# Optimization experiments

Hardware: AMD Instinct MI355X
Metric: run time of the kernel (lower is better)

## Reference

```python
import jax, jax.numpy as jnp
import numpy as np

H, DK = 16, 64
F = H * DK  # n_feat = 1024
B, T = 2, 2048


def setup_inputs() -> dict:
    key = jax.random.key(0)
    ks = jax.random.split(key, 11)
    mk = lambda k, sh: jax.random.normal(k, sh, dtype=jnp.float32)
    inp = {
        "query": mk(ks[0], (B, T, F)),
        "key": mk(ks[1], (B, T, F)),
        "value": mk(ks[2], (B, T, F)),
    }
    # Standard RoPE frequency table, shaped [T,1,1,DK] to broadcast over [t,b,h,d].
    pos = jnp.arange(T, dtype=jnp.float32)[:, None]
    inv_freq = 1.0 / (10000.0 ** (jnp.arange(0, DK, 2, dtype=jnp.float32) / DK))
    ang = pos * inv_freq                       # [T, DK/2]
    emb = jnp.concatenate([ang, ang], axis=-1)  # [T, DK]
    inp["cos"] = jnp.cos(emb)[:, None, None, :]
    inp["sin"] = jnp.sin(emb)[:, None, None, :]
    scale = 1.0 / np.sqrt(F).astype(np.float32)
    for i, n in enumerate(["wq", "wk", "wv", "wo"]):
        inp[n] = mk(ks[3 + i], (F, F)) * scale  # torch Linear weight layout [out,in]
    for i, n in enumerate(["bq", "bk", "bv", "bo"]):
        inp[n] = mk(ks[7 + i], (F,)) * 0.01
    return inp


def _rtt_half(x):
    d = x.shape[-1]
    return jnp.concatenate([-x[..., d // 2:], x[..., :d // 2]], axis=-1)


def reference(query, key, value, cos, sin, wq, bq, wk, bk, wv, bv, wo, bo):
    b, t, f = query.shape
    h, d = H, DK
    # [b,t,f] -> [t,b,h,d] as in the torch code (RoPE applied pre-projection)
    to_tbhd = lambda x: jnp.swapaxes(x, 0, 1).reshape(t, b, h, d)
    q = to_tbhd(query)
    k = to_tbhd(key)
    c, s = cos[:t], sin[:t]
    q = q * c + _rtt_half(q) * s
    k = k * c + _rtt_half(k) * s
    back = lambda x: jnp.swapaxes(x.reshape(t, b, f), 0, 1)  # -> [b,t,f]
    q, k = back(q), back(k)
    lin = lambda x, w, bias: x @ w.T + bias
    Q = lin(q, wq, bq).reshape(b, t, h, d)
    K = lin(k, wk, bk).reshape(b, t, h, d)
    V = lin(value, wv, bv).reshape(b, t, h, d)
    scores = jnp.einsum('bqhd,bkhd->bhqk', Q, K) / jnp.sqrt(jnp.float32(d))
    attn = jax.nn.softmax(scores, axis=-1)
    o = jnp.einsum('bhqk,bkhd->bqhd', attn, V).reshape(b, t, f)
    return o @ wo.T + bo
```

## Files before the change

### kernel.cpp

```cpp
#include <hip/hip_runtime.h>
#include <hip/hip_bf16.h>

#define DEVI __device__ __forceinline__

typedef unsigned short u16;
typedef unsigned int u32;
typedef __attribute__((ext_vector_type(8))) short bf16x8;
typedef __attribute__((ext_vector_type(4))) short bf16x4;
typedef __attribute__((ext_vector_type(4))) float f32x4;

#define Bn 2
#define Tn 2048
#define Hn 16
#define Dn 64
#define Fn 1024

DEVI u16 tobf(float f) {
    __hip_bfloat16 h = __float2bfloat16(f);
    return __builtin_bit_cast(u16, h);
}
DEVI float frombf(u16 u) {
    return __builtin_bit_cast(float, ((u32)u) << 16);
}

DEVI f32x4 mfma16(bf16x8 a, bf16x8 b, f32x4 c) {
    return __builtin_amdgcn_mfma_f32_16x16x32_bf16(a, b, c, 0, 0, 0);
}

DEVI void gload_lds16(const u16* g, u16* l) {
    __builtin_amdgcn_global_load_lds(
        (const __attribute__((address_space(1))) void*)g,
        (__attribute__((address_space(3))) void*)l, 16, 0, 0);
}

__global__ __launch_bounds__(256) void k_prep(const float* __restrict__ q,
                                              const float* __restrict__ k,
                                              const float* __restrict__ v,
                                              const float* __restrict__ cosb,
                                              const float* __restrict__ sinb,
                                              const float* __restrict__ wq,
                                              const float* __restrict__ wk,
                                              const float* __restrict__ wv,
                                              const float* __restrict__ wo,
                                              u16* __restrict__ Aq,
                                              u16* __restrict__ Ak,
                                              u16* __restrict__ Av) {
    if (blockIdx.x < 4096) {
        unsigned idx = blockIdx.x * 256 + threadIdx.x;
        unsigned which = idx >> 19;
        unsigned r = idx & 0x7FFFFu;
        unsigned d0 = (r & 7u) << 2;
        unsigned h = (r >> 3) & 15u;
        unsigned t = (r >> 7) & 2047u;
        unsigned b = (r >> 18) & 1u;
        const float* src = which ? k : q;
        u16* dst = which ? Ak : Aq;
        size_t base = ((size_t)(b * Tn + t)) * Fn + h * Dn;
        float4 lo = *(const float4*)(src + base + d0);
        float4 hi = *(const float4*)(src + base + d0 + 32);
        float4 cl = *(const float4*)(cosb + (size_t)t * Dn + d0);
        float4 ch = *(const float4*)(cosb + (size_t)t * Dn + d0 + 32);
        float4 sl = *(const float4*)(sinb + (size_t)t * Dn + d0);
        float4 sh = *(const float4*)(sinb + (size_t)t * Dn + d0 + 32);
        bf16x4 olo, ohi;
        olo[0] = (short)tobf(lo.x * cl.x - hi.x * sl.x);
        olo[1] = (short)tobf(lo.y * cl.y - hi.y * sl.y);
        olo[2] = (short)tobf(lo.z * cl.z - hi.z * sl.z);
        olo[3] = (short)tobf(lo.w * cl.w - hi.w * sl.w);
        ohi[0] = (short)tobf(hi.x * ch.x + lo.x * sh.x);
        ohi[1] = (short)tobf(hi.y * ch.y + lo.y * sh.y);
        ohi[2] = (short)tobf(hi.z * ch.z + lo.z * sh.z);
        ohi[3] = (short)tobf(hi.w * ch.w + lo.w * sh.w);
        *(bf16x4*)(dst + base + d0) = olo;
        *(bf16x4*)(dst + base + d0 + 32) = ohi;
    } else {
        size_t i8 = (((size_t)blockIdx.x - 4096) * 256 + threadIdx.x) * 8;
        const size_t M4 = (size_t)4 << 20, M1 = (size_t)1 << 20;
        const float* src;
        size_t off;
        if (i8 < M4)              { src = v;  off = i8; }
        else if (i8 < M4 + M1)    { src = wq; off = i8 - M4; }
        else if (i8 < M4 + 2*M1)  { src = wk; off = i8 - M4 - M1; }
        else if (i8 < M4 + 3*M1)  { src = wv; off = i8 - M4 - 2*M1; }
        else                      { src = wo; off = i8 - M4 - 3*M1; }
        float4 a = *(const float4*)(src + off);
        float4 c = *(const float4*)(src + off + 4);
        bf16x8 vv;
        vv[0] = (short)tobf(a.x); vv[1] = (short)tobf(a.y);
        vv[2] = (short)tobf(a.z); vv[3] = (short)tobf(a.w);
        vv[4] = (short)tobf(c.x); vv[5] = (short)tobf(c.y);
        vv[6] = (short)tobf(c.z); vv[7] = (short)tobf(c.w);
        *(bf16x8*)(Av + i8) = vv;
    }
}

DEVI void store_out(u16* p, float v) { *p = tobf(v); }
DEVI void store_out(float* p, float v) { *p = v; }

template <typename OUT>
DEVI void gemm_body(const u16* __restrict__ A, const u16* __restrict__ W,
                    const float* __restrict__ bias, OUT* __restrict__ C,
                    float scale, u16* As, u16* Bs, int mode) {
    const int tid = threadIdx.x;
    const int lane = tid & 63;
    const int wave = tid >> 6;
    const int l15 = lane & 15, l4 = lane >> 4;
    const int id = blockIdx.x + (blockIdx.y << 3);
    const int swz = ((id & 7) << 5) + (id >> 3);
    const int bn = (swz & 7) << 7, bm = (swz >> 3) << 7;
    const int wr = (wave >> 1) << 6, wc = (wave & 1) << 6;

    const int c0 = tid, c1 = tid + 256;
    const int r0 = c0 >> 2, r1 = c1 >> 2;
    const int cc0 = (((c0 & 3) ^ ((r0 >> 1) & 3)) << 3);
    const int cc1 = (((c1 & 3) ^ ((r1 >> 1) & 3)) << 3);
    const u16* A0p = A + (size_t)(bm + r0) * 1024 + cc0;
    const u16* A1p = A + (size_t)(bm + r1) * 1024 + cc1;
    const u16* B0p = W + (size_t)(bn + r0) * 1024 + cc0;
    const u16* B1p = W + (size_t)(bn + r1) * 1024 + cc1;
    u16* Ad0 = As + (c0 << 3);
    u16* Ad1 = As + (c1 << 3);
    u16* Bd0 = Bs + (c0 << 3);
    u16* Bd1 = Bs + (c1 << 3);

    const int gsw = (l15 >> 1) & 3;
    const int fco = ((l4 ^ gsw) << 3);

    f32x4 acc[4][4] = {};

    for (int k0 = 0; k0 < 1024; k0 += 32) {
        gload_lds16(A0p + k0, Ad0);
        gload_lds16(A1p + k0, Ad1);
        gload_lds16(B0p + k0, Bd0);
        gload_lds16(B1p + k0, Bd1);
        __syncthreads();
        bf16x8 af[4], bfr[4];
        #pragma unroll
        for (int m = 0; m < 4; m++)
            af[m] = *(const bf16x8*)(As + (wr + m * 16 + l15) * 32 + fco);
        #pragma unroll
        for (int n = 0; n < 4; n++)
            bfr[n] = *(const bf16x8*)(Bs + (wc + n * 16 + l15) * 32 + fco);
        #pragma unroll
        for (int m = 0; m < 4; m++)
            #pragma unroll
            for (int n = 0; n < 4; n++)
                acc[m][n] = mfma16(af[m], bfr[n], acc[m][n]);
        __syncthreads();
    }

    #pragma unroll
    for (int m = 0; m < 4; m++)
        #pragma unroll
        for (int n = 0; n < 4; n++) {
            const int gcol = bn + wc + n * 16 + l15;
            const float bb = bias[gcol];
            #pragma unroll
            for (int j = 0; j < 4; j++) {
                const int grow = bm + wr + m * 16 + (l4 << 2) + j;
                const float val = (acc[m][n][j] + bb) * scale;
                if (mode == 0) {
                    store_out(C + (size_t)grow * 1024 + gcol, val);
                } else {
                    const int b = grow >> 11, t = grow & 2047;
                    const int h = gcol >> 6, d = gcol & 63;
                    const int bh = b * 16 + h, tt2 = t >> 6, r = t & 63;
                    const size_t tbase = ((size_t)(bh * 32 + tt2)) << 12;
                    size_t off;
                    if (mode == 1) {
                        const int nn = ((r >> 5) << 1) | ((r >> 2) & 1);
                        const int kk = d >> 5, ll4 = (d >> 3) & 3, e = d & 7;
                        const int ll15 = (((r >> 3) & 3) << 2) | (r & 3);
                        off = tbase + ((size_t)(nn * 2 + kk) << 9) +
                              ((ll4 * 16 + ll15) << 3) + e;
                    } else {
                        const int kk = r >> 5, ll4 = (r >> 3) & 3, e = r & 7;
                        const int nd = d >> 4, ll15 = d & 15;
                        off = tbase + ((size_t)(kk * 4 + nd) << 9) +
                              ((ll4 * 16 + ll15) << 3) + e;
                    }
                    ((u16*)C)[off] = tobf(val);
                }
            }
        }
}

__global__ __launch_bounds__(256) void k_gemm_qkv(
    const u16* A0, const u16* W0, const float* b0, u16* C0,
    const u16* A1, const u16* W1, const float* b1, u16* C1,
    const u16* A2, const u16* W2, const float* b2, u16* C2) {
    __shared__ __align__(16) u16 As[128 * 32];
    __shared__ __align__(16) u16 Bs[128 * 32];
    const int z = blockIdx.z;
    const u16* A = z == 0 ? A0 : (z == 1 ? A1 : A2);
    const u16* W = z == 0 ? W0 : (z == 1 ? W1 : W2);
    const float* bias = z == 0 ? b0 : (z == 1 ? b1 : b2);
    u16* C = z == 0 ? C0 : (z == 1 ? C1 : C2);
    const float scale = z == 0 ? 0.125f * 1.4426950408889634f : 1.0f;
    gemm_body<u16>(A, W, bias, C, scale, As, Bs, z);
}

__global__ __launch_bounds__(256) void k_gemm_f32(const u16* __restrict__ A,
                                                  const u16* __restrict__ W,
                                                  const float* __restrict__ bias,
                                                  float* __restrict__ C) {
    __shared__ __align__(16) u16 As[128 * 32];
    __shared__ __align__(16) u16 Bs[128 * 32];
    gemm_body<float>(A, W, bias, C, 1.0f, As, Bs, 0);
}

__global__ __launch_bounds__(256) void k_attn(const u16* __restrict__ Qp,
                                              const u16* __restrict__ Kr,
                                              const u16* __restrict__ Vr,
                                              u16* __restrict__ Op0,
                                              u16* __restrict__ Op1,
                                              float* __restrict__ Ls) {
    __shared__ __align__(16) u16 Ks[2][4096];
    __shared__ __align__(16) u16 Vs[2][4096];
    const int tid = threadIdx.x, wave = tid >> 6, lane = tid & 63;
    const int l15 = lane & 15, l4 = lane >> 4;
    const int bh = blockIdx.x, b = bh >> 4, h = bh & 15;
    const int sp = blockIdx.z;
    const int q0 = blockIdx.y * 128 + wave * 32;
    const int tbase = sp << 4;

    bf16x8 aq[2][2];
    #pragma unroll
    for (int mq = 0; mq < 2; mq++)
        #pragma unroll
        for (int kk = 0; kk < 2; kk++)
            aq[mq][kk] = *(const bf16x8*)(Qp +
                ((size_t)(b * Tn + q0 + mq * 16 + l15)) * Fn + h * Dn + kk * 32 + (l4 << 3));

    f32x4 o[2][4] = {};
    f32x4 osum[2] = {};
    const f32x4 zero4 = {0.f, 0.f, 0.f, 0.f};

    bf16x8 ones;
    #pragma unroll
    for (int j = 0; j < 8; j++) ones[j] = (short)0x3F80;

    const u16* Kbr = Kr + ((size_t)bh << 17);
    const u16* Vbr = Vr + ((size_t)bh << 17);
    const int lo8 = lane * 8;

    #define STAGE(bf, tg)                                                     \
        _Pragma("unroll")                                                     \
        for (int i = 0; i < 2; i++) {                                         \
            const int c = wave + i * 4;                                       \
            gload_lds16(Kbr + (((tg) * 8 + c) << 9) + lo8,                    \
                        &Ks[bf][(c << 9) + lo8]);                             \
            gload_lds16(Vbr + (((tg) * 8 + c) << 9) + lo8,                    \
                        &Vs[bf][(c << 9) + lo8]);                             \
        }

    STAGE(0, tbase);
    __syncthreads();
    int cur = 0;

    #pragma unroll 1
    for (int tt = 0; tt < 16; tt++) {
        if (tt < 15) STAGE(cur ^ 1, tbase + tt + 1);

        bf16x8 ka[4][2], va[2][4];
        #pragma unroll
        for (int n = 0; n < 4; n++)
            #pragma unroll
            for (int kk = 0; kk < 2; kk++)
                ka[n][kk] = *(const bf16x8*)(&Ks[cur][((n * 2 + kk) << 9) + lo8]);
        #pragma unroll
        for (int kk = 0; kk < 2; kk++)
            #pragma unroll
            for (int nd = 0; nd < 4; nd++)
                va[kk][nd] = *(const bf16x8*)(&Vs[cur][((kk * 4 + nd) << 9) + lo8]);

        f32x4 s[2][4];
        __builtin_amdgcn_s_setprio(1);
        #pragma unroll
        for (int n = 0; n < 4; n++) {
            s[0][n] = mfma16(ka[n][0], aq[0][0], zero4);
            s[1][n] = mfma16(ka[n][0], aq[1][0], zero4);
            s[0][n] = mfma16(ka[n][1], aq[0][1], s[0][n]);
            s[1][n] = mfma16(ka[n][1], aq[1][1], s[1][n]);
        }
        __builtin_amdgcn_s_setprio(0);

        bf16x8 pb[2][2];
        #pragma unroll
        for (int mq = 0; mq < 2; mq++)
            #pragma unroll
            for (int kk = 0; kk < 2; kk++) {
                float p0 = __builtin_amdgcn_exp2f(s[mq][2 * kk][0]);
                float p1 = __builtin_amdgcn_exp2f(s[mq][2 * kk][1]);
                float p2 = __builtin_amdgcn_exp2f(s[mq][2 * kk][2]);
                float p3 = __builtin_amdgcn_exp2f(s[mq][2 * kk][3]);
                float p4 = __builtin_amdgcn_exp2f(s[mq][2 * kk + 1][0]);
                float p5 = __builtin_amdgcn_exp2f(s[mq][2 * kk + 1][1]);
                float p6 = __builtin_amdgcn_exp2f(s[mq][2 * kk + 1][2]);
                float p7 = __builtin_amdgcn_exp2f(s[mq][2 * kk + 1][3]);
                bf16x8 pv;
                pv[0] = (short)tobf(p0); pv[1] = (short)tobf(p1);
                pv[2] = (short)tobf(p2); pv[3] = (short)tobf(p3);
                pv[4] = (short)tobf(p4); pv[5] = (short)tobf(p5);
                pv[6] = (short)tobf(p6); pv[7] = (short)tobf(p7);
                pb[mq][kk] = pv;
            }

        __builtin_amdgcn_s_setprio(1);
        osum[0] = mfma16(ones, pb[0][0], osum[0]);
        osum[1] = mfma16(ones, pb[1][0], osum[1]);
        osum[0] = mfma16(ones, pb[0][1], osum[0]);
        osum[1] = mfma16(ones, pb[1][1], osum[1]);
        #pragma unroll
        for (int kk = 0; kk < 2; kk++)
            #pragma unroll
            for (int nd = 0; nd < 4; nd++) {
                o[0][nd] = mfma16(va[kk][nd], pb[0][kk], o[0][nd]);
                o[1][nd] = mfma16(va[kk][nd], pb[1][kk], o[1][nd]);
            }
        __builtin_amdgcn_s_setprio(0);

        __syncthreads();
        cur ^= 1;
    }
    #undef STAGE

    u16* OpS = sp ? Op1 : Op0;
    #pragma unroll
    for (int mq = 0; mq < 2; mq++) {
        const int q = q0 + mq * 16 + l15;
        const float lsum = osum[mq][0];
        float inv = 1.f / lsum;
        #pragma unroll
        for (int nd = 0; nd < 4; nd++) {
            bf16x4 ov;
            ov[0] = (short)tobf(o[mq][nd][0] * inv);
            ov[1] = (short)tobf(o[mq][nd][1] * inv);
            ov[2] = (short)tobf(o[mq][nd][2] * inv);
            ov[3] = (short)tobf(o[mq][nd][3] * inv);
            *(bf16x4*)(OpS + ((size_t)(b * Tn + q)) * Fn +
                       h * Dn + nd * 16 + (l4 << 2)) = ov;
        }
        if (l4 == 0)
            Ls[(((size_t)(sp * 2 + b)) * Tn + q) * Hn + h] = lsum;
    }
}

__global__ __launch_bounds__(256) void k_combine(const u16* __restrict__ Op0,
                                                 const u16* __restrict__ Op1,
                                                 const float* __restrict__ Ls,
                                                 u16* __restrict__ Oa) {
    size_t e0 = ((size_t)blockIdx.x * 256 + threadIdx.x) * 8;
    int row = (int)(e0 >> 10);
    int b = row >> 11, q = row & 2047;
    int h = (int)(e0 >> 6) & 15;
    float l0 = Ls[(((size_t)(0 + b)) * Tn + q) * Hn + h];
    float l1 = Ls[(((size_t)(2 + b)) * Tn + q) * Hn + h];
    float inv = 1.f / (l0 + l1);
    float w0 = l0 * inv, w1 = l1 * inv;
    bf16x8 x0 = *(const bf16x8*)(Op0 + e0);
    bf16x8 x1 = *(const bf16x8*)(Op1 + e0);
    bf16x8 out;
    #pragma unroll
    for (int j = 0; j < 8; j++)
        out[j] = (short)tobf(frombf((u16)x0[j]) * w0 + frombf((u16)x1[j]) * w1);
    *(bf16x8*)(Oa + e0) = out;
}

extern "C" void kernel_launch(void* const* d_in, const int* in_sizes, int n_in,
                              void* d_out, int out_size, void* d_ws, size_t ws_size,
                              hipStream_t stream) {
    const float* q    = (const float*)d_in[0];
    const float* k    = (const float*)d_in[1];
    const float* v    = (const float*)d_in[2];
    const float* cosb = (const float*)d_in[3];
    const float* sinb = (const float*)d_in[4];
    const float* wq   = (const float*)d_in[5];
    const float* wk   = (const float*)d_in[6];
    const float* wv   = (const float*)d_in[7];
    const float* wo   = (const float*)d_in[8];
    const float* bq   = (const float*)d_in[9];
    const float* bk   = (const float*)d_in[10];
    const float* bv   = (const float*)d_in[11];
    const float* bo   = (const float*)d_in[12];

    char* ws = (char*)d_ws;
    char* dob = (char*)d_out;
    const size_t MB = (size_t)1 << 20;
    u16* Aq  = (u16*)(ws);
    u16* Ak  = (u16*)(ws + 8 * MB);
    u16* Av  = (u16*)(ws + 16 * MB);
    u16* Wq  = (u16*)(ws + 24 * MB);
    u16* Wk  = (u16*)(ws + 26 * MB);
    u16* Wv  = (u16*)(ws + 28 * MB);
    u16* Wo  = (u16*)(ws + 30 * MB);
    u16* Qp  = (u16*)(ws + 32 * MB);
    u16* Kr  = (u16*)(ws + 40 * MB);
    u16* Vr  = (u16*)(ws + 48 * MB);
    u16* Op0 = (u16*)(dob);
    u16* Op1 = (u16*)(dob + 8 * MB);
    float* Ls = (float*)(ws + 16 * MB);
    u16* Oa  = (u16*)(ws);

    k_prep<<<8192, 256, 0, stream>>>(q, k, v, cosb, sinb, wq, wk, wv, wo,
                                     Aq, Ak, Av);
    k_gemm_qkv<<<dim3(8, 32, 3), 256, 0, stream>>>(Aq, Wq, bq, Qp,
                                                   Ak, Wk, bk, Kr,
                                                   Av, Wv, bv, Vr);
    k_attn<<<dim3(32, 16, 2), 256, 0, stream>>>(Qp, Kr, Vr, Op0, Op1, Ls);
    k_combine<<<2048, 256, 0, stream>>>(Op0, Op1, Ls, Oa);
    k_gemm_f32<<<dim3(8, 32), 256, 0, stream>>>(Oa, Wo, bo, (float*)d_out);
}
```

Measured before the change: 128.1 us.

## Drop split-KV attention and combine kernel, process full key range per block

Attention blocks now iterate over all 32 key tiles instead of splitting the key range in two across blockIdx.z. This removes the partial-output writes, the row-sum buffer and the separate combine kernel launch with its extra memory traffic. In exchange the grid shrinks from 1024 to 512 blocks, each doing twice the serial work, which lowers parallelism and occupancy on a many-CU GPU.

```diff
diff --git a/kernel.cpp b/kernel.cpp
--- a/kernel.cpp
+++ b/kernel.cpp
@@ -212,17 +212,13 @@
 __global__ __launch_bounds__(256) void k_attn(const u16* __restrict__ Qp,
                                               const u16* __restrict__ Kr,
                                               const u16* __restrict__ Vr,
-                                              u16* __restrict__ Op0,
-                                              u16* __restrict__ Op1,
-                                              float* __restrict__ Ls) {
+                                              u16* __restrict__ Oa) {
     __shared__ __align__(16) u16 Ks[2][4096];
     __shared__ __align__(16) u16 Vs[2][4096];
     const int tid = threadIdx.x, wave = tid >> 6, lane = tid & 63;
     const int l15 = lane & 15, l4 = lane >> 4;
     const int bh = blockIdx.x, b = bh >> 4, h = bh & 15;
-    const int sp = blockIdx.z;
     const int q0 = blockIdx.y * 128 + wave * 32;
-    const int tbase = sp << 4;
 
     bf16x8 aq[2][2];
     #pragma unroll
@@ -254,13 +250,13 @@
                         &Vs[bf][(c << 9) + lo8]);                             \
         }
 
-    STAGE(0, tbase);
+    STAGE(0, 0);
     __syncthreads();
     int cur = 0;
 
     #pragma unroll 1
-    for (int tt = 0; tt < 16; tt++) {
-        if (tt < 15) STAGE(cur ^ 1, tbase + tt + 1);
+    for (int tt = 0; tt < 32; tt++) {
+        if (tt < 31) STAGE(cur ^ 1, tt + 1);
 
         bf16x8 ka[4][2], va[2][4];
         #pragma unroll
@@ -325,12 +321,10 @@
     }
     #undef STAGE
 
-    u16* OpS = sp ? Op1 : Op0;
     #pragma unroll
     for (int mq = 0; mq < 2; mq++) {
         const int q = q0 + mq * 16 + l15;
-        const float lsum = osum[mq][0];
-        float inv = 1.f / lsum;
+        float inv = 1.f / osum[mq][0];
         #pragma unroll
         for (int nd = 0; nd < 4; nd++) {
             bf16x4 ov;
@@ -338,33 +332,10 @@
             ov[1] = (short)tobf(o[mq][nd][1] * inv);
             ov[2] = (short)tobf(o[mq][nd][2] * inv);
             ov[3] = (short)tobf(o[mq][nd][3] * inv);
-            *(bf16x4*)(OpS + ((size_t)(b * Tn + q)) * Fn +
+            *(bf16x4*)(Oa + ((size_t)(b * Tn + q)) * Fn +
                        h * Dn + nd * 16 + (l4 << 2)) = ov;
         }
-        if (l4 == 0)
-            Ls[(((size_t)(sp * 2 + b)) * Tn + q) * Hn + h] = lsum;
     }
-}
-
-__global__ __launch_bounds__(256) void k_combine(const u16* __restrict__ Op0,
-                                                 const u16* __restrict__ Op1,
-                                                 const float* __restrict__ Ls,
-                                                 u16* __restrict__ Oa) {
-    size_t e0 = ((size_t)blockIdx.x * 256 + threadIdx.x) * 8;
-    int row = (int)(e0 >> 10);
-    int b = row >> 11, q = row & 2047;
-    int h = (int)(e0 >> 6) & 15;
-    float l0 = Ls[(((size_t)(0 + b)) * Tn + q) * Hn + h];
-    float l1 = Ls[(((size_t)(2 + b)) * Tn + q) * Hn + h];
-    float inv = 1.f / (l0 + l1);
-    float w0 = l0 * inv, w1 = l1 * inv;
-    bf16x8 x0 = *(const bf16x8*)(Op0 + e0);
-    bf16x8 x1 = *(const bf16x8*)(Op1 + e0);
-    bf16x8 out;
-    #pragma unroll
-    for (int j = 0; j < 8; j++)
-        out[j] = (short)tobf(frombf((u16)x0[j]) * w0 + frombf((u16)x1[j]) * w1);
-    *(bf16x8*)(Oa + e0) = out;
 }
 
 extern "C" void kernel_launch(void* const* d_in, const int* in_sizes, int n_in,
@@ -385,7 +356,6 @@
     const float* bo   = (const float*)d_in[12];
 
     char* ws = (char*)d_ws;
-    char* dob = (char*)d_out;
     const size_t MB = (size_t)1 << 20;
     u16* Aq  = (u16*)(ws);
     u16* Ak  = (u16*)(ws + 8 * MB);
@@ -397,17 +367,13 @@
     u16* Qp  = (u16*)(ws + 32 * MB);
     u16* Kr  = (u16*)(ws + 40 * MB);
     u16* Vr  = (u16*)(ws + 48 * MB);
-    u16* Op0 = (u16*)(dob);
-    u16* Op1 = (u16*)(dob + 8 * MB);
-    float* Ls = (float*)(ws + 16 * MB);
-    u16* Oa  = (u16*)(ws);
+    u16* Oa  = Aq;
 
     k_prep<<<8192, 256, 0, stream>>>(q, k, v, cosb, sinb, wq, wk, wv, wo,
                                      Aq, Ak, Av);
     k_gemm_qkv<<<dim3(8, 32, 3), 256, 0, stream>>>(Aq, Wq, bq, Qp,
                                                    Ak, Wk, bk, Kr,
                                                    Av, Wv, bv, Vr);
-    k_attn<<<dim3(32, 16, 2), 256, 0, stream>>>(Qp, Kr, Vr, Op0, Op1, Ls);
-    k_combine<<<2048, 256, 0, stream>>>(Op0, Op1, Ls, Oa);
+    k_attn<<<dim3(32, 16), 256, 0, stream>>>(Qp, Kr, Vr, Oa);
     k_gemm_f32<<<dim3(8, 32), 256, 0, stream>>>(Oa, Wo, bo, (float*)d_out);
 }
```

Measured after the change: 118.7 us, median of 2. 7.3% less time.
